# Optimization experiments

Hardware: AMD Instinct MI355X
Metric: run time of the kernel (lower is better)

The kernel has to match this reference:

```python
import jax, jax.numpy as jnp
import numpy as np

EPS = 1e-3  # Keras LayerNormalization default epsilon


def layernorm(x, g, b):
    mu = jnp.mean(x, axis=-1, keepdims=True)
    var = jnp.var(x, axis=-1, keepdims=True)
    return (x - mu) * jax.lax.rsqrt(var + EPS) * g + b


def setup_inputs() -> dict:
    key = jax.random.key(0)
    ks = jax.random.split(key, 16)
    B, T, C = 2, 2048, 1024
    F = 4 * C
    std = 0.02
    inp = {
        "x": jax.random.normal(ks[0], (B, T, C), jnp.float32),
        "ln1_g": jnp.ones((C,), jnp.float32),
        "ln1_b": jnp.zeros((C,), jnp.float32),
        "Wq": std * jax.random.normal(ks[1], (C, C), jnp.float32),
        "bq": jnp.zeros((C,), jnp.float32),
        "Wk": std * jax.random.normal(ks[2], (C, C), jnp.float32),
        "bk": jnp.zeros((C,), jnp.float32),
        "Wv": std * jax.random.normal(ks[3], (C, C), jnp.float32),
        "bv": jnp.zeros((C,), jnp.float32),
        "ln2_g": jnp.ones((C,), jnp.float32),
        "ln2_b": jnp.zeros((C,), jnp.float32),
        "W1": std * jax.random.normal(ks[4], (C, F), jnp.float32),
        "b1": jnp.zeros((F,), jnp.float32),
        "W2": std * jax.random.normal(ks[5], (F, C), jnp.float32),
        "b2": jnp.zeros((C,), jnp.float32),
    }
    return inp


N_HEADS = 16


def reference(x, ln1_g, ln1_b, Wq, bq, Wk, bk, Wv, bv, ln2_g, ln2_b, W1, b1, W2, b2):
    B, T, C = x.shape
    H = N_HEADS
    D = C // H

    h = layernorm(x, ln1_g, ln1_b)
    # [B,T,C] -> [B,H,T,D]
    def split_heads(y):
        return y.reshape(B, T, H, D).transpose(0, 2, 1, 3)

    q = split_heads(h @ Wq + bq)
    k = split_heads(h @ Wk + bk)
    v = split_heads(h @ Wv + bv)

    # Faithful to original: scores = K @ Q^T, i.e. scores[i,j] = k_i . q_j
    scores = jnp.einsum("bhid,bhjd->bhij", k, q) / jnp.sqrt(jnp.float32(D))
    causal = jnp.tril(jnp.ones((T, T), bool))  # [T,T]
    scores = jnp.where(causal[None, None], scores, -jnp.inf)
    w = jax.nn.softmax(scores, axis=-1)
    attn = jnp.einsum("bhij,bhjd->bhid", w, v)  # [B,H,T,D]
    attn = attn.transpose(0, 2, 1, 3).reshape(B, T, C)
    x = x + attn

    h2 = layernorm(x, ln2_g, ln2_b)
    ffn = jax.nn.gelu(h2 @ W1 + b1, approximate=False) @ W2 + b2
    x = x + ffn
    return x
```

## Files before the change

kernel.cpp:

```cpp
#include <hip/hip_runtime.h>
#include <hip/hip_bf16.h>
#include <math.h>

typedef __hip_bfloat16 bf16;
typedef __attribute__((ext_vector_type(8))) short bf16x8;
typedef __attribute__((ext_vector_type(4))) float f32x4;

__device__ __forceinline__ unsigned short f2bf_rne(float f) {
  unsigned u = __float_as_uint(f);
  u += 0x7fffu + ((u >> 16) & 1u);
  return (unsigned short)(u >> 16);
}
__device__ __forceinline__ float bf2f(unsigned short s) {
  return __uint_as_float(((unsigned)s) << 16);
}

__device__ __forceinline__ float gelu_fast(float v) {
  float u = v * (0.7978845608f + 0.0356774081f * v * v);
  float t = __builtin_amdgcn_exp2f(u * 2.8853900818f);
  float r = __builtin_amdgcn_rcpf(t + 1.0f);
  return v - v * r;
}

#define GLOBAL_AS __attribute__((address_space(1)))
#define LDS_AS __attribute__((address_space(3)))
__device__ __forceinline__ void gl2lds16(const void* g, void* l) {
  __builtin_amdgcn_global_load_lds((const GLOBAL_AS void*)g, (LDS_AS void*)l, 16, 0, 0);
}

__device__ __forceinline__ int swz8(int f, int nwg) {
  return (f & 7) * (nwg >> 3) + (f >> 3);
}

#define SCALE_CS 0.18033688011112042f

__device__ __forceinline__ void ln_body(const float* __restrict__ x,
                                        const float* __restrict__ g,
                                        const float* __restrict__ b,
                                        bf16* __restrict__ h, int row, int t) {
  const float4 xv = ((const float4*)(x + (size_t)row * 1024))[t];
  float s = xv.x + xv.y + xv.z + xv.w;
  float sq = xv.x * xv.x + xv.y * xv.y + xv.z * xv.z + xv.w * xv.w;
  #pragma unroll
  for (int m = 1; m < 64; m <<= 1) { s += __shfl_xor(s, m); sq += __shfl_xor(sq, m); }
  __shared__ float ps[4], pq[4];
  if ((t & 63) == 0) { ps[t >> 6] = s; pq[t >> 6] = sq; }
  __syncthreads();
  s = ps[0] + ps[1] + ps[2] + ps[3];
  sq = pq[0] + pq[1] + pq[2] + pq[3];
  float mean = s * (1.0f / 1024.0f);
  float var = sq * (1.0f / 1024.0f) - mean * mean;
  float rs = rsqrtf(var + 1e-3f);
  float4 gv = ((const float4*)g)[t];
  float4 bv = ((const float4*)b)[t];
  ushort4 o;
  o.x = f2bf_rne((xv.x - mean) * rs * gv.x + bv.x);
  o.y = f2bf_rne((xv.y - mean) * rs * gv.y + bv.y);
  o.z = f2bf_rne((xv.z - mean) * rs * gv.z + bv.z);
  o.w = f2bf_rne((xv.w - mean) * rs * gv.w + bv.w);
  ((ushort4*)(h + (size_t)row * 1024))[t] = o;
}

__global__ __launch_bounds__(256) void ln_kernel(const float* __restrict__ x,
                                                 const float* __restrict__ g,
                                                 const float* __restrict__ b,
                                                 bf16* __restrict__ h) {
  ln_body(x, g, b, h, blockIdx.x, threadIdx.x);
}

__device__ __forceinline__ void tr_tile(const float* __restrict__ W, bf16* __restrict__ WT,
                                        int R, int Cc, int bx, int by, int t) {
  __shared__ float tile[32][33];
  int tx = t & 31, ty = t >> 5;
  #pragma unroll
  for (int k = 0; k < 4; k++) {
    int rr = ty + k * 8;
    tile[rr][tx] = W[(size_t)(by + rr) * Cc + bx + tx];
  }
  __syncthreads();
  unsigned short* out = reinterpret_cast<unsigned short*>(WT);
  #pragma unroll
  for (int k = 0; k < 4; k++) {
    int rr = ty + k * 8;
    out[(size_t)(bx + rr) * R + by + tx] = f2bf_rne(tile[tx][rr]);
  }
}

__global__ __launch_bounds__(256) void prep_fused(const float* __restrict__ x,
                                                  const float* __restrict__ ln1g,
                                                  const float* __restrict__ ln1b,
                                                  bf16* __restrict__ h,
                                                  const float* __restrict__ Wq,
                                                  const float* __restrict__ Wk,
                                                  const float* __restrict__ Wv,
                                                  const float* __restrict__ W1,
                                                  const float* __restrict__ W2,
                                                  bf16* __restrict__ WqkT,
                                                  bf16* __restrict__ W1T,
                                                  bf16* __restrict__ W2T) {
  int id = blockIdx.x, t = threadIdx.x;
  if (id < 4096) { ln_body(x, ln1g, ln1b, h, id, t); return; }
  id -= 4096;
  if (id < 3072) {
    int sect = id >> 10, r = id & 1023;
    const float* W = sect == 0 ? Wq : (sect == 1 ? Wk : Wv);
    bf16* WT = WqkT + (size_t)sect * 1048576;
    tr_tile(W, WT, 1024, 1024, (r & 31) * 32, (r >> 5) * 32, t);
  } else if (id < 7168) {
    int r = id - 3072;
    tr_tile(W1, W1T, 1024, 4096, (r & 127) * 32, (r >> 7) * 32, t);
  } else {
    int r = id - 7168;
    tr_tile(W2, W2T, 4096, 1024, (r & 31) * 32, (r >> 5) * 32, t);
  }
}

__device__ __forceinline__ void mainloop_256(const bf16* __restrict__ A,
                                             const bf16* __restrict__ BT,
                                             int lda, int nk, int m0, int n0,
                                             char* ldsb, int t,
                                             f32x4 (&acc)[8][4]) {
  const int lane = t & 63, wave = t >> 6;
  const int l = lane & 15, quad = lane >> 4;
  const int wm = (wave >> 2) * 128, wn = (wave & 3) * 64;
  const int srow = wave * 8 + (lane >> 3);
  const int scol = ((lane & 7) ^ (lane >> 3)) * 8;
  const int grp0 = (quad ^ (l & 7)) * 16;
  const int grp1 = ((4 + quad) ^ (l & 7)) * 16;

  bf16x8 a[4][2], b01[2][2], b23[2][2];

  auto stA = [&](int buf, int half, int kt) {
    const bf16* s = A + (size_t)(m0 + half * 128 + srow) * lda + kt * 64 + scol;
    char* d = ldsb + buf * 65536 + half * 16384 + wave * 1024;
    gl2lds16(s, d);
    gl2lds16(s + (size_t)64 * lda, d + 8192);
  };
  auto stB = [&](int buf, int half, int kt) {
    const bf16* s = BT + (size_t)(n0 + half * 128 + srow) * lda + kt * 64 + scol;
    char* d = ldsb + buf * 65536 + 32768 + half * 16384 + wave * 1024;
    gl2lds16(s, d);
    gl2lds16(s + (size_t)64 * lda, d + 8192);
  };
  auto rdA = [&](int buf, int mh) {
    const char* base = ldsb + buf * 65536 + (wm + mh * 64 + l) * 128;
    #pragma unroll
    for (int ii = 0; ii < 4; ii++) {
      a[ii][0] = *(const bf16x8*)(base + ii * 2048 + grp0);
      a[ii][1] = *(const bf16x8*)(base + ii * 2048 + grp1);
    }
  };
  auto rdB = [&](int buf, int nh, bf16x8 (&bb)[2][2]) {
    const char* base = ldsb + buf * 65536 + 32768 + (wn + nh * 32 + l) * 128;
    #pragma unroll
    for (int jj = 0; jj < 2; jj++) {
      bb[jj][0] = *(const bf16x8*)(base + jj * 2048 + grp0);
      bb[jj][1] = *(const bf16x8*)(base + jj * 2048 + grp1);
    }
  };
  auto mm4 = [&](int mi, bf16x8 (&bb)[2][2], int nj) {
    #pragma unroll
    for (int ii = 0; ii < 4; ii++)
      #pragma unroll
      for (int jj = 0; jj < 2; jj++) {
        acc[mi + ii][nj + jj] = __builtin_amdgcn_mfma_f32_16x16x32_bf16(
            a[ii][0], bb[jj][0], acc[mi + ii][nj + jj], 0, 0, 0);
        acc[mi + ii][nj + jj] = __builtin_amdgcn_mfma_f32_16x16x32_bf16(
            a[ii][1], bb[jj][1], acc[mi + ii][nj + jj], 0, 0, 0);
      }
  };

#define BARX() __builtin_amdgcn_s_barrier()
#define LGKM0() do { asm volatile("s_waitcnt lgkmcnt(0)" ::: "memory"); \
                     __builtin_amdgcn_sched_barrier(0); } while (0)
#define HALF4(BC, DOA, SAB, SAK, DOB, SBB, SBK, VMN)                      \
  do {                                                                    \
    rdA(BC, 0); rdB(BC, 0, b01);                                          \
    if (DOA) stA(SAB, 0, SAK);                                            \
    BARX(); LGKM0();                                                      \
    __builtin_amdgcn_s_setprio(1); mm4(0, b01, 0);                        \
    __builtin_amdgcn_s_setprio(0); BARX();                                \
    rdB(BC, 1, b23);                                                      \
    if (DOA) stA(SAB, 1, SAK);                                            \
    BARX(); LGKM0();                                                      \
    __builtin_amdgcn_s_setprio(1); mm4(0, b23, 2);                        \
    __builtin_amdgcn_s_setprio(0); BARX();                                \
    rdA(BC, 1);                                                           \
    if (DOB) stB(SBB, 0, SBK);                                            \
    BARX(); LGKM0();                                                      \
    __builtin_amdgcn_s_setprio(1); mm4(4, b01, 0);                        \
    __builtin_amdgcn_s_setprio(0); BARX();                                \
    if (DOB) stB(SBB, 1, SBK);                                            \
    BARX();                                                               \
    __builtin_amdgcn_s_setprio(1); mm4(4, b23, 2);                        \
    __builtin_amdgcn_s_setprio(0);                                        \
    asm volatile("s_waitcnt vmcnt(" VMN ")" ::: "memory");                \
    BARX();                                                               \
  } while (0)

  const int nt = nk >> 6;
  stA(0, 0, 0); stA(0, 1, 0);
  stB(0, 0, 0); stB(0, 1, 0);
  stB(1, 0, 1); stB(1, 1, 1);
  asm volatile("s_waitcnt vmcnt(4)" ::: "memory");
  BARX();
  int tt = 0;
  for (; tt + 2 < nt; tt += 2) {
    HALF4(0, 1, 1, tt + 1, 1, 0, tt + 2, "4");
    HALF4(1, 1, 0, tt + 2, 1, 1, tt + 3, "4");
  }
  HALF4(0, 1, 1, tt + 1, 0, 0, 0, "0");
  HALF4(1, 0, 0, 0, 0, 0, 0, "0");
#undef HALF4
#undef LGKM0
#undef BARX
}

__global__ __launch_bounds__(512, 2) void gemm_ffn1(const bf16* __restrict__ A,
                                                    const bf16* __restrict__ BT,
                                                    const float* __restrict__ bias,
                                                    bf16* __restrict__ out,
                                                    int N, int K) {
  extern __shared__ char lds[];
  int t = threadIdx.x;
  int nf = swz8(blockIdx.x, gridDim.x);
  int n0 = (nf & 15) * 256, m0 = (nf >> 4) * 256;
  f32x4 acc[8][4];
  #pragma unroll
  for (int i = 0; i < 8; i++)
    #pragma unroll
    for (int j = 0; j < 4; j++) acc[i][j] = (f32x4){0.f, 0.f, 0.f, 0.f};
  mainloop_256(A, BT, K, K, m0, n0, lds, t, acc);

  int lane = t & 63, wave = t >> 6;
  int l = lane & 15, quad = lane >> 4;
  int wm = (wave >> 2) * 128, wn = (wave & 3) * 64;
  int r4 = quad * 4;
  unsigned short* os = reinterpret_cast<unsigned short*>(out);
  #pragma unroll
  for (int i = 0; i < 8; i++)
    #pragma unroll
    for (int j = 0; j < 4; j++) {
      int col = n0 + wn + j * 16 + l;
      float bval = bias[col];
      #pragma unroll
      for (int r = 0; r < 4; r++) {
        int row = m0 + wm + i * 16 + r4 + r;
        os[(size_t)row * N + col] = f2bf_rne(gelu_fast(acc[i][j][r] + bval));
      }
    }
}

__global__ __launch_bounds__(512, 2) void gemm_ffn2(const bf16* __restrict__ A,
                                                    const bf16* __restrict__ BT,
                                                    unsigned short* __restrict__ p0,
                                                    unsigned short* __restrict__ p1,
                                                    unsigned short* __restrict__ p2,
                                                    unsigned short* __restrict__ p3) {
  extern __shared__ char lds[];
  int t = threadIdx.x;
  int nf = swz8(blockIdx.x, gridDim.x);
  int n0 = (nf & 3) * 256, m0 = ((nf >> 2) & 15) * 256;
  int z = nf >> 6;
  f32x4 acc[8][4];
  #pragma unroll
  for (int i = 0; i < 8; i++)
    #pragma unroll
    for (int j = 0; j < 4; j++) acc[i][j] = (f32x4){0.f, 0.f, 0.f, 0.f};
  mainloop_256(A + z * 1024, BT + z * 1024, 4096, 1024, m0, n0, lds, t, acc);

  unsigned short* p = z == 0 ? p0 : (z == 1 ? p1 : (z == 2 ? p2 : p3));
  int lane = t & 63, wave = t >> 6;
  int l = lane & 15, quad = lane >> 4;
  int wm = (wave >> 2) * 128, wn = (wave & 3) * 64;
  int r4 = quad * 4;
  #pragma unroll
  for (int i = 0; i < 8; i++)
    #pragma unroll
    for (int j = 0; j < 4; j++) {
      int col = n0 + wn + j * 16 + l;
      #pragma unroll
      for (int r = 0; r < 4; r++) {
        int row = m0 + wm + i * 16 + r4 + r;
        p[(size_t)row * 1024 + col] = f2bf_rne(acc[i][j][r]);
      }
    }
}

__global__ __launch_bounds__(256) void reduce_ffn2(const unsigned short* __restrict__ p0,
                                                   const unsigned short* __restrict__ p1,
                                                   const unsigned short* __restrict__ p2,
                                                   const unsigned short* __restrict__ p3,
                                                   const float* __restrict__ x1,
                                                   const float* __restrict__ bias,
                                                   float* __restrict__ out) {
  int row = blockIdx.x, t = threadIdx.x;
  size_t base = (size_t)row * 1024;
  ushort4 a = ((const ushort4*)(p0 + base))[t];
  ushort4 b = ((const ushort4*)(p1 + base))[t];
  ushort4 c = ((const ushort4*)(p2 + base))[t];
  ushort4 d = ((const ushort4*)(p3 + base))[t];
  float4 xv = ((const float4*)(x1 + base))[t];
  float4 bv = ((const float4*)bias)[t];
  float4 o;
  o.x = (bf2f(a.x) + bf2f(b.x)) + (bf2f(c.x) + bf2f(d.x)) + xv.x + bv.x;
  o.y = (bf2f(a.y) + bf2f(b.y)) + (bf2f(c.y) + bf2f(d.y)) + xv.y + bv.y;
  o.z = (bf2f(a.z) + bf2f(b.z)) + (bf2f(c.z) + bf2f(d.z)) + xv.z + bv.z;
  o.w = (bf2f(a.w) + bf2f(b.w)) + (bf2f(c.w) + bf2f(d.w)) + xv.w + bv.w;
  ((float4*)(out + base))[t] = o;
}

__global__ __launch_bounds__(512, 2) void gemm_qkv(const bf16* __restrict__ A,
                                                   const bf16* __restrict__ BT,
                                                   const float* __restrict__ bq,
                                                   const float* __restrict__ bk,
                                                   const float* __restrict__ bv,
                                                   bf16* __restrict__ qb,
                                                   bf16* __restrict__ kb,
                                                   bf16* __restrict__ vt,
                                                   int K) {
  extern __shared__ char lds[];
  int t = threadIdx.x;
  int nf = swz8(blockIdx.x, gridDim.x);
  int n0 = (nf % 12) * 256, m0 = (nf / 12) * 256;
  f32x4 acc[8][4];
  #pragma unroll
  for (int i = 0; i < 8; i++)
    #pragma unroll
    for (int j = 0; j < 4; j++) acc[i][j] = (f32x4){0.f, 0.f, 0.f, 0.f};
  mainloop_256(A, BT, K, K, m0, n0, lds, t, acc);

  int lane = t & 63, wave = t >> 6;
  int l = lane & 15, quad = lane >> 4;
  int wm = (wave >> 2) * 128, wn = (wave & 3) * 64;
  int sect = n0 >> 10;
  const float* bias = sect == 0 ? bq : (sect == 1 ? bk : bv);
  int r4 = quad * 4;
  if (sect < 2) {
    bf16* o = sect == 0 ? qb : kb;
    unsigned short* os = reinterpret_cast<unsigned short*>(o);
    float scl = sect == 1 ? SCALE_CS : 1.0f;
    #pragma unroll
    for (int i = 0; i < 8; i++)
      #pragma unroll
      for (int j = 0; j < 4; j++) {
        int col = n0 + wn + j * 16 + l;
        int c1 = col & 1023;
        float bval = bias[c1];
        int row0 = m0 + wm + i * 16 + r4;
        #pragma unroll
        for (int r = 0; r < 4; r++)
          os[(size_t)(row0 + r) * 1024 + c1] = f2bf_rne((acc[i][j][r] + bval) * scl);
      }
  } else {
    unsigned short* Ls = (unsigned short*)lds;
    #pragma unroll
    for (int i = 0; i < 8; i++)
      #pragma unroll
      for (int j = 0; j < 4; j++) {
        int c1l = wn + j * 16 + l;
        float bval = bias[(n0 - 2048) + c1l];
        ushort4 pk;
        pk.x = f2bf_rne(acc[i][j][0] + bval);
        pk.y = f2bf_rne(acc[i][j][1] + bval);
        pk.z = f2bf_rne(acc[i][j][2] + bval);
        pk.w = f2bf_rne(acc[i][j][3] + bval);
        int gq = ((wm + i * 16) >> 2) + quad;
        *(ushort4*)((char*)Ls + c1l * 512 + ((gq ^ (c1l & 15)) << 3)) = pk;
      }
    __syncthreads();
    int bb = m0 >> 11, t0b = m0 & 2047;
    size_t vbase = ((size_t)(bb * 1024 + (n0 - 2048))) * 2048 + t0b;
    #pragma unroll 4
    for (int it2 = 0; it2 < 32; it2++) {
      int c1row = it2 * 8 + wave;
      uint2 v = *(const uint2*)((char*)Ls + c1row * 512 +
                                ((lane ^ (c1row & 15)) << 3));
      *(uint2*)((unsigned short*)vt + vbase + (size_t)c1row * 2048 + lane * 4) = v;
    }
  }
}

__global__ __launch_bounds__(512, 4) void attn_mfma(const bf16* __restrict__ qb,
                                                    const bf16* __restrict__ kb,
                                                    const bf16* __restrict__ vt,
                                                    const float* __restrict__ x,
                                                    float* __restrict__ x1) {
  extern __shared__ char alds[];
  char* KVb = alds;
  char* Pb  = alds + 65536;
  int t = threadIdx.x;
  int nf = swz8(blockIdx.x, 1024);
  int chunk = nf >> 7, local = nf & 127;
  int y = local >> 2;
  int bh = chunk * 4 + (local & 3);
  int b = bh >> 4, h = bh & 15;
  size_t qk_base = (size_t)b * 2048 * 1024 + (size_t)h * 64;
  size_t vt_base = (size_t)bh * 64 * 2048;
  int lane = t & 63, wave = t >> 6;
  int g = wave >> 2, w4 = wave & 3;
  int l = lane & 15, quad = lane >> 4;
  int sw = l & 7;
  int srow8 = lane >> 3;
  int scol = ((lane & 7) ^ srow8) * 8;
  int it = 31 - y;
  int i0 = it * 64;
  int njt = it + 1;
  int iblk = i0 + w4 * 16;

  bf16x8 ones;
  #pragma unroll
  for (int z = 0; z < 8; z++) ones[z] = (short)0x3F80;

  if (g == 0) {
    #pragma unroll
    for (int c = 0; c < 2; c++) {
      int rr = w4 * 16 + c * 8 + srow8;
      gl2lds16(kb + qk_base + (size_t)(i0 + rr) * 1024 + scol,
               Pb + w4 * 2048 + c * 1024);
      gl2lds16(qb + qk_base + (size_t)rr * 1024 + scol,
               KVb + w4 * 2048 + c * 1024);
      gl2lds16(vt + vt_base + (size_t)rr * 2048 + scol,
               KVb + 8192 + w4 * 2048 + c * 1024);
    }
  } else if (njt > 1) {
    #pragma unroll
    for (int c = 0; c < 2; c++) {
      int rr = w4 * 16 + c * 8 + srow8;
      gl2lds16(qb + qk_base + (size_t)(64 + rr) * 1024 + scol,
               KVb + 32768 + w4 * 2048 + c * 1024);
      gl2lds16(vt + vt_base + (size_t)rr * 2048 + 64 + scol,
               KVb + 32768 + 8192 + w4 * 2048 + c * 1024);
    }
  }
  __syncthreads();

  const char* qr = Pb + w4 * 2048 + l * 128;
  bf16x8 qf0 = *(const bf16x8*)(qr + ((quad ^ sw) * 16));
  bf16x8 qf1 = *(const bf16x8*)(qr + (((4 + quad) ^ sw) * 16));
  __syncthreads();

  f32x4 Oacc[4], Ol;
  #pragma unroll
  for (int dt = 0; dt < 4; dt++) Oacc[dt] = (f32x4){0.f, 0.f, 0.f, 0.f};
  Ol = (f32x4){0.f, 0.f, 0.f, 0.f};

  char* Pw = Pb + wave * 2048 + l * 128;
  char* KVg = KVb + g * 32768;
  int nstep = (njt + 1) >> 1;
  int buf = 0;
  for (int s = 0; s < nstep; s++) {
    int jt = 2 * s + g;
    if (jt + 2 < njt) {
      int j1 = (jt + 2) * 64;
      #pragma unroll
      for (int c = 0; c < 2; c++) {
        int rr = w4 * 16 + c * 8 + srow8;
        gl2lds16(qb + qk_base + (size_t)(j1 + rr) * 1024 + scol,
                 KVg + (buf ^ 1) * 16384 + w4 * 2048 + c * 1024);
        gl2lds16(vt + vt_base + (size_t)rr * 2048 + j1 + scol,
                 KVg + (buf ^ 1) * 16384 + 8192 + w4 * 2048 + c * 1024);
      }
    }
    if (jt < njt) {
      int j0v = jt * 64;
      const bf16* Kb = (const bf16*)(KVg + buf * 16384);
      #pragma unroll
      for (int nt = 0; nt < 4; nt++) {
        int jb = j0v + nt * 16;
        uint2 pk;
        if (jb > iblk + 15) {
          pk.x = 0u; pk.y = 0u;
        } else {
          const bf16* kr = Kb + (nt * 16 + l) * 64;
          bf16x8 kf0 = *(const bf16x8*)(kr + ((quad ^ sw) * 8));
          bf16x8 kf1 = *(const bf16x8*)(kr + (((4 + quad) ^ sw) * 8));
          f32x4 sv = (f32x4){0.f, 0.f, 0.f, 0.f};
          sv = __builtin_amdgcn_mfma_f32_16x16x32_bf16(kf0, qf0, sv, 0, 0, 0);
          sv = __builtin_amdgcn_mfma_f32_16x16x32_bf16(kf1, qf1, sv, 0, 0, 0);
          float p0, p1, p2, p3;
          if (jb + 15 <= iblk) {
            p0 = __builtin_amdgcn_exp2f(sv[0]);
            p1 = __builtin_amdgcn_exp2f(sv[1]);
            p2 = __builtin_amdgcn_exp2f(sv[2]);
            p3 = __builtin_amdgcn_exp2f(sv[3]);
          } else {
            int i_ = iblk + l, jbase = jb + quad * 4;
            p0 = (jbase + 0 > i_) ? 0.f : __builtin_amdgcn_exp2f(sv[0]);
            p1 = (jbase + 1 > i_) ? 0.f : __builtin_amdgcn_exp2f(sv[1]);
            p2 = (jbase + 2 > i_) ? 0.f : __builtin_amdgcn_exp2f(sv[2]);
            p3 = (jbase + 3 > i_) ? 0.f : __builtin_amdgcn_exp2f(sv[3]);
          }
          union { __hip_bfloat162 h2; unsigned u; } c0u, c1u;
          c0u.h2 = __float22bfloat162_rn(make_float2(p0, p1));
          c1u.h2 = __float22bfloat162_rn(make_float2(p2, p3));
          pk.x = c0u.u; pk.y = c1u.u;
        }
        *(uint2*)(Pw + (((nt * 2 + (quad >> 1)) ^ sw) << 4) + ((quad & 1) << 3)) = pk;
      }
      asm volatile("s_waitcnt lgkmcnt(0)" ::: "memory");

      bf16x8 ap0 = *(const bf16x8*)(Pw + ((quad ^ sw) << 4));
      bf16x8 ap1 = *(const bf16x8*)(Pw + (((4 + quad) ^ sw) << 4));
      const bf16* Vb = (const bf16*)(KVg + buf * 16384 + 8192);
      #pragma unroll
      for (int dt = 0; dt < 4; dt++) {
        const bf16* vr = Vb + (dt * 16 + l) * 64;
        bf16x8 bv0 = *(const bf16x8*)(vr + ((quad ^ sw) * 8));
        bf16x8 bv1 = *(const bf16x8*)(vr + (((4 + quad) ^ sw) * 8));
        Oacc[dt] = __builtin_amdgcn_mfma_f32_16x16x32_bf16(ap0, bv0, Oacc[dt], 0, 0, 0);
        Oacc[dt] = __builtin_amdgcn_mfma_f32_16x16x32_bf16(ap1, bv1, Oacc[dt], 0, 0, 0);
      }
      Ol = __builtin_amdgcn_mfma_f32_16x16x32_bf16(ap0, ones, Ol, 0, 0, 0);
      Ol = __builtin_amdgcn_mfma_f32_16x16x32_bf16(ap1, ones, Ol, 0, 0, 0);
    }
    __syncthreads();
    buf ^= 1;
  }

  float* F = (float*)KVb;
  int fbase = w4 * 1280;
  if (g == 1) {
    #pragma unroll
    for (int dt = 0; dt < 4; dt++)
      #pragma unroll
      for (int r = 0; r < 4; r++)
        F[fbase + (dt * 4 + r) * 64 + lane] = Oacc[dt][r];
    #pragma unroll
    for (int r = 0; r < 4; r++)
      F[fbase + 1024 + r * 64 + lane] = Ol[r];
  }
  __syncthreads();
  if (g == 0) {
    #pragma unroll
    for (int dt = 0; dt < 4; dt++)
      #pragma unroll
      for (int r = 0; r < 4; r++)
        Oacc[dt][r] += F[fbase + (dt * 4 + r) * 64 + lane];
    #pragma unroll
    for (int r = 0; r < 4; r++)
      Ol[r] += F[fbase + 1024 + r * 64 + lane];
    #pragma unroll
    for (int r = 0; r < 4; r++) {
      float inv = 1.0f / Ol[r];
      int row = iblk + quad * 4 + r;
      size_t gi = qk_base + (size_t)row * 1024;
      #pragma unroll
      for (int dt = 0; dt < 4; dt++) {
        int d = dt * 16 + l;
        x1[gi + d] = x[gi + d] + Oacc[dt][r] * inv;
      }
    }
  }
}

extern "C" void kernel_launch(void* const* d_in, const int* in_sizes, int n_in,
                              void* d_out, int out_size, void* d_ws, size_t ws_size,
                              hipStream_t stream) {
  const float* x    = (const float*)d_in[0];
  const float* ln1g = (const float*)d_in[1];
  const float* ln1b = (const float*)d_in[2];
  const float* Wq   = (const float*)d_in[3];
  const float* bq   = (const float*)d_in[4];
  const float* Wk   = (const float*)d_in[5];
  const float* bk   = (const float*)d_in[6];
  const float* Wv   = (const float*)d_in[7];
  const float* bv   = (const float*)d_in[8];
  const float* ln2g = (const float*)d_in[9];
  const float* ln2b = (const float*)d_in[10];
  const float* W1   = (const float*)d_in[11];
  const float* b1   = (const float*)d_in[12];
  const float* W2   = (const float*)d_in[13];
  const float* b2   = (const float*)d_in[14];

  char* ws = (char*)d_ws;
  float* x1  = (float*)(ws + 0);
  bf16* h    = (bf16*)(ws + 16777216);
  bf16* WqkT = (bf16*)(ws + 25165824);
  bf16* W1T  = (bf16*)(ws + 31457280);
  bf16* W2T  = (bf16*)(ws + 39845888);
  bf16* qb   = (bf16*)(ws + 48234496);
  bf16* kb   = (bf16*)(ws + 56623104);
  bf16* vt   = (bf16*)(ws + 65011712);
  bf16* act  = (bf16*)(ws + 73400320);

  static bool s_attr_done = false;
  if (!s_attr_done) {
    hipFuncSetAttribute(reinterpret_cast<const void*>(gemm_qkv),
                        hipFuncAttributeMaxDynamicSharedMemorySize, 131072);
    hipFuncSetAttribute(reinterpret_cast<const void*>(gemm_ffn1),
                        hipFuncAttributeMaxDynamicSharedMemorySize, 131072);
    hipFuncSetAttribute(reinterpret_cast<const void*>(gemm_ffn2),
                        hipFuncAttributeMaxDynamicSharedMemorySize, 131072);
    hipFuncSetAttribute(reinterpret_cast<const void*>(attn_mfma),
                        hipFuncAttributeMaxDynamicSharedMemorySize, 81920);
    s_attr_done = true;
  }

  prep_fused<<<15360, 256, 0, stream>>>(x, ln1g, ln1b, h,
                                        Wq, Wk, Wv, W1, W2, WqkT, W1T, W2T);
  gemm_qkv<<<192, 512, 131072, stream>>>(h, WqkT, bq, bk, bv, qb, kb, vt, 1024);
  attn_mfma<<<1024, 512, 81920, stream>>>(qb, kb, vt, x, x1);
  ln_kernel<<<4096, 256, 0, stream>>>(x1, ln2g, ln2b, h);
  gemm_ffn1<<<256, 512, 131072, stream>>>(h, W1T, b1, act, 4096, 1024);
  gemm_ffn2<<<256, 512, 131072, stream>>>(act, W2T,
      (unsigned short*)qb, (unsigned short*)kb, (unsigned short*)vt, (unsigned short*)h);
  reduce_ffn2<<<4096, 256, 0, stream>>>((const unsigned short*)qb, (const unsigned short*)kb,
                                        (const unsigned short*)vt, (const unsigned short*)h,
                                        x1, b2, (float*)d_out);
}
```

Baseline: 276.4 us.

## Use 256x128 tiles with split-K 2 for FFN2 instead of split-K 4

```diff
diff --git a/kernel.cpp b/kernel.cpp
--- a/kernel.cpp
+++ b/kernel.cpp
@@ -216,6 +216,101 @@
 #undef BARX
 }
 
+__device__ __forceinline__ void mainloop_256x128(const bf16* __restrict__ A,
+                                                 const bf16* __restrict__ BT,
+                                                 int lda, int nk, int m0, int n0,
+                                                 char* ldsb, int t,
+                                                 f32x4 (&acc)[8][2]) {
+  const int lane = t & 63, wave = t >> 6;
+  const int l = lane & 15, quad = lane >> 4;
+  const int wm = (wave >> 2) * 128, wn = (wave & 3) * 32;
+  const int srow = wave * 8 + (lane >> 3);
+  const int scol = ((lane & 7) ^ (lane >> 3)) * 8;
+  const int grp0 = (quad ^ (l & 7)) * 16;
+  const int grp1 = ((4 + quad) ^ (l & 7)) * 16;
+
+  bf16x8 a[4][2], bb[2][2];
+
+  auto stA = [&](int buf, int half, int kt) {
+    const bf16* s = A + (size_t)(m0 + half * 128 + srow) * lda + kt * 64 + scol;
+    char* d = ldsb + buf * 49152 + half * 16384 + wave * 1024;
+    gl2lds16(s, d);
+    gl2lds16(s + (size_t)64 * lda, d + 8192);
+  };
+  auto stB = [&](int buf, int kt) {
+    const bf16* s = BT + (size_t)(n0 + srow) * lda + kt * 64 + scol;
+    char* d = ldsb + buf * 49152 + 32768 + wave * 1024;
+    gl2lds16(s, d);
+    gl2lds16(s + (size_t)64 * lda, d + 8192);
+  };
+  auto rdA = [&](int buf, int mh) {
+    const char* base = ldsb + buf * 49152 + (wm + mh * 64 + l) * 128;
+    #pragma unroll
+    for (int ii = 0; ii < 4; ii++) {
+      a[ii][0] = *(const bf16x8*)(base + ii * 2048 + grp0);
+      a[ii][1] = *(const bf16x8*)(base + ii * 2048 + grp1);
+    }
+  };
+  auto rdB = [&](int buf) {
+    const char* base = ldsb + buf * 49152 + 32768 + (wn + l) * 128;
+    #pragma unroll
+    for (int jj = 0; jj < 2; jj++) {
+      bb[jj][0] = *(const bf16x8*)(base + jj * 2048 + grp0);
+      bb[jj][1] = *(const bf16x8*)(base + jj * 2048 + grp1);
+    }
+  };
+  auto mm = [&](int mi) {
+    #pragma unroll
+    for (int ii = 0; ii < 4; ii++)
+      #pragma unroll
+      for (int jj = 0; jj < 2; jj++) {
+        acc[mi + ii][jj] = __builtin_amdgcn_mfma_f32_16x16x32_bf16(
+            a[ii][0], bb[jj][0], acc[mi + ii][jj], 0, 0, 0);
+        acc[mi + ii][jj] = __builtin_amdgcn_mfma_f32_16x16x32_bf16(
+            a[ii][1], bb[jj][1], acc[mi + ii][jj], 0, 0, 0);
+      }
+  };
+
+#define BARX() __builtin_amdgcn_s_barrier()
+#define LGKM0() do { asm volatile("s_waitcnt lgkmcnt(0)" ::: "memory"); \
+                     __builtin_amdgcn_sched_barrier(0); } while (0)
+  const int nt = nk >> 6;
+  stB(0, 0);
+  stA(0, 0, 0); stA(0, 1, 0);
+  stB(1, 1);
+  asm volatile("s_waitcnt vmcnt(2)" ::: "memory");
+  BARX();
+  for (int T = 0; T < nt; T += 2) {
+    int lastm = (T + 2 >= nt);
+    rdA(0, 0); rdB(0);
+    stA(1, 0, T + 1); stA(1, 1, T + 1);
+    BARX(); LGKM0();
+    __builtin_amdgcn_s_setprio(1); mm(0); __builtin_amdgcn_s_setprio(0);
+    BARX();
+    rdA(0, 1);
+    if (!lastm) stB(0, T + 2);
+    BARX(); LGKM0();
+    __builtin_amdgcn_s_setprio(1); mm(4); __builtin_amdgcn_s_setprio(0);
+    if (!lastm) asm volatile("s_waitcnt vmcnt(2)" ::: "memory");
+    else        asm volatile("s_waitcnt vmcnt(0)" ::: "memory");
+    BARX();
+    rdA(1, 0); rdB(1);
+    if (!lastm) { stA(0, 0, T + 2); stA(0, 1, T + 2); }
+    BARX(); LGKM0();
+    __builtin_amdgcn_s_setprio(1); mm(0); __builtin_amdgcn_s_setprio(0);
+    BARX();
+    rdA(1, 1);
+    if (!lastm) stB(1, T + 3);
+    BARX(); LGKM0();
+    __builtin_amdgcn_s_setprio(1); mm(4); __builtin_amdgcn_s_setprio(0);
+    if (!lastm) asm volatile("s_waitcnt vmcnt(2)" ::: "memory");
+    else        asm volatile("s_waitcnt vmcnt(0)" ::: "memory");
+    BARX();
+  }
+#undef LGKM0
+#undef BARX
+}
+
 __global__ __launch_bounds__(512, 2) void gemm_ffn1(const bf16* __restrict__ A,
                                                     const bf16* __restrict__ BT,
                                                     const float* __restrict__ bias,
@@ -254,30 +349,28 @@
 __global__ __launch_bounds__(512, 2) void gemm_ffn2(const bf16* __restrict__ A,
                                                     const bf16* __restrict__ BT,
                                                     unsigned short* __restrict__ p0,
-                                                    unsigned short* __restrict__ p1,
-                                                    unsigned short* __restrict__ p2,
-                                                    unsigned short* __restrict__ p3) {
+                                                    unsigned short* __restrict__ p1) {
   extern __shared__ char lds[];
   int t = threadIdx.x;
   int nf = swz8(blockIdx.x, gridDim.x);
-  int n0 = (nf & 3) * 256, m0 = ((nf >> 2) & 15) * 256;
-  int z = nf >> 6;
-  f32x4 acc[8][4];
+  int n0 = (nf & 7) * 128, m0 = ((nf >> 3) & 15) * 256;
+  int z = nf >> 7;
+  f32x4 acc[8][2];
   #pragma unroll
   for (int i = 0; i < 8; i++)
     #pragma unroll
-    for (int j = 0; j < 4; j++) acc[i][j] = (f32x4){0.f, 0.f, 0.f, 0.f};
-  mainloop_256(A + z * 1024, BT + z * 1024, 4096, 1024, m0, n0, lds, t, acc);
-
-  unsigned short* p = z == 0 ? p0 : (z == 1 ? p1 : (z == 2 ? p2 : p3));
+    for (int j = 0; j < 2; j++) acc[i][j] = (f32x4){0.f, 0.f, 0.f, 0.f};
+  mainloop_256x128(A + z * 2048, BT + z * 2048, 4096, 2048, m0, n0, lds, t, acc);
+
+  unsigned short* p = z ? p1 : p0;
   int lane = t & 63, wave = t >> 6;
   int l = lane & 15, quad = lane >> 4;
-  int wm = (wave >> 2) * 128, wn = (wave & 3) * 64;
+  int wm = (wave >> 2) * 128, wn = (wave & 3) * 32;
   int r4 = quad * 4;
   #pragma unroll
   for (int i = 0; i < 8; i++)
     #pragma unroll
-    for (int j = 0; j < 4; j++) {
+    for (int j = 0; j < 2; j++) {
       int col = n0 + wn + j * 16 + l;
       #pragma unroll
       for (int r = 0; r < 4; r++) {
@@ -289,8 +382,6 @@
 
 __global__ __launch_bounds__(256) void reduce_ffn2(const unsigned short* __restrict__ p0,
                                                    const unsigned short* __restrict__ p1,
-                                                   const unsigned short* __restrict__ p2,
-                                                   const unsigned short* __restrict__ p3,
                                                    const float* __restrict__ x1,
                                                    const float* __restrict__ bias,
                                                    float* __restrict__ out) {
@@ -298,15 +389,13 @@
   size_t base = (size_t)row * 1024;
   ushort4 a = ((const ushort4*)(p0 + base))[t];
   ushort4 b = ((const ushort4*)(p1 + base))[t];
-  ushort4 c = ((const ushort4*)(p2 + base))[t];
-  ushort4 d = ((const ushort4*)(p3 + base))[t];
   float4 xv = ((const float4*)(x1 + base))[t];
   float4 bv = ((const float4*)bias)[t];
   float4 o;
-  o.x = (bf2f(a.x) + bf2f(b.x)) + (bf2f(c.x) + bf2f(d.x)) + xv.x + bv.x;
-  o.y = (bf2f(a.y) + bf2f(b.y)) + (bf2f(c.y) + bf2f(d.y)) + xv.y + bv.y;
-  o.z = (bf2f(a.z) + bf2f(b.z)) + (bf2f(c.z) + bf2f(d.z)) + xv.z + bv.z;
-  o.w = (bf2f(a.w) + bf2f(b.w)) + (bf2f(c.w) + bf2f(d.w)) + xv.w + bv.w;
+  o.x = (bf2f(a.x) + bf2f(b.x)) + xv.x + bv.x;
+  o.y = (bf2f(a.y) + bf2f(b.y)) + xv.y + bv.y;
+  o.z = (bf2f(a.z) + bf2f(b.z)) + xv.z + bv.z;
+  o.w = (bf2f(a.w) + bf2f(b.w)) + xv.w + bv.w;
   ((float4*)(out + base))[t] = o;
 }
 
@@ -591,7 +680,7 @@
     hipFuncSetAttribute(reinterpret_cast<const void*>(gemm_ffn1),
                         hipFuncAttributeMaxDynamicSharedMemorySize, 131072);
     hipFuncSetAttribute(reinterpret_cast<const void*>(gemm_ffn2),
-                        hipFuncAttributeMaxDynamicSharedMemorySize, 131072);
+                        hipFuncAttributeMaxDynamicSharedMemorySize, 98304);
     hipFuncSetAttribute(reinterpret_cast<const void*>(attn_mfma),
                         hipFuncAttributeMaxDynamicSharedMemorySize, 81920);
     s_attr_done = true;
@@ -603,9 +692,8 @@
   attn_mfma<<<1024, 512, 81920, stream>>>(qb, kb, vt, x, x1);
   ln_kernel<<<4096, 256, 0, stream>>>(x1, ln2g, ln2b, h);
   gemm_ffn1<<<256, 512, 131072, stream>>>(h, W1T, b1, act, 4096, 1024);
-  gemm_ffn2<<<256, 512, 131072, stream>>>(act, W2T,
-      (unsigned short*)qb, (unsigned short*)kb, (unsigned short*)vt, (unsigned short*)h);
+  gemm_ffn2<<<256, 512, 98304, stream>>>(act, W2T,
+      (unsigned short*)qb, (unsigned short*)kb);
   reduce_ffn2<<<4096, 256, 0, stream>>>((const unsigned short*)qb, (const unsigned short*)kb,
-                                        (const unsigned short*)vt, (const unsigned short*)h,
                                         x1, b2, (float*)d_out);
 }
```

Result: no change. 275.8 us (-0.2%).

## Replace split-K FFN2 with 128x128 full-K tiles and fused residual epilogue

Applied to the files above, without the earlier changes.

```diff
diff --git a/kernel.cpp b/kernel.cpp
--- a/kernel.cpp
+++ b/kernel.cpp
@@ -216,6 +216,81 @@
 #undef BARX
 }
 
+__device__ __forceinline__ void mainloop_128(const bf16* __restrict__ A,
+                                             const bf16* __restrict__ BT,
+                                             int lda, int nk, int m0, int n0,
+                                             char* ldsb, int t,
+                                             f32x4 (&acc)[4][2]) {
+  const int lane = t & 63, wave = t >> 6;
+  const int l = lane & 15, quad = lane >> 4;
+  const int wm = (wave >> 2) * 64, wn = (wave & 3) * 32;
+  const int srow = wave * 8 + (lane >> 3);
+  const int scol = ((lane & 7) ^ (lane >> 3)) * 8;
+  const int grp0 = (quad ^ (l & 7)) * 16;
+  const int grp1 = ((4 + quad) ^ (l & 7)) * 16;
+
+  bf16x8 a[4][2], bb[2][2];
+
+  auto stage = [&](int buf, int kt) {
+    const bf16* sa = A + (size_t)(m0 + srow) * lda + kt * 64 + scol;
+    char* da = ldsb + buf * 32768 + wave * 1024;
+    gl2lds16(sa, da);
+    gl2lds16(sa + (size_t)64 * lda, da + 8192);
+    const bf16* sb = BT + (size_t)(n0 + srow) * lda + kt * 64 + scol;
+    char* db = ldsb + buf * 32768 + 16384 + wave * 1024;
+    gl2lds16(sb, db);
+    gl2lds16(sb + (size_t)64 * lda, db + 8192);
+  };
+  auto rd = [&](int buf) {
+    const char* ab = ldsb + buf * 32768 + (wm + l) * 128;
+    #pragma unroll
+    for (int ii = 0; ii < 4; ii++) {
+      a[ii][0] = *(const bf16x8*)(ab + ii * 2048 + grp0);
+      a[ii][1] = *(const bf16x8*)(ab + ii * 2048 + grp1);
+    }
+    const char* bbase = ldsb + buf * 32768 + 16384 + (wn + l) * 128;
+    #pragma unroll
+    for (int jj = 0; jj < 2; jj++) {
+      bb[jj][0] = *(const bf16x8*)(bbase + jj * 2048 + grp0);
+      bb[jj][1] = *(const bf16x8*)(bbase + jj * 2048 + grp1);
+    }
+  };
+  auto mm = [&]() {
+    #pragma unroll
+    for (int ii = 0; ii < 4; ii++)
+      #pragma unroll
+      for (int jj = 0; jj < 2; jj++) {
+        acc[ii][jj] = __builtin_amdgcn_mfma_f32_16x16x32_bf16(
+            a[ii][0], bb[jj][0], acc[ii][jj], 0, 0, 0);
+        acc[ii][jj] = __builtin_amdgcn_mfma_f32_16x16x32_bf16(
+            a[ii][1], bb[jj][1], acc[ii][jj], 0, 0, 0);
+      }
+  };
+
+#define BARX() __builtin_amdgcn_s_barrier()
+#define LGKM0() do { asm volatile("s_waitcnt lgkmcnt(0)" ::: "memory"); \
+                     __builtin_amdgcn_sched_barrier(0); } while (0)
+  const int nt = nk >> 6;
+  stage(0, 0);
+  stage(1, 1);
+  asm volatile("s_waitcnt vmcnt(4)" ::: "memory");
+  BARX();
+  int buf = 0;
+  for (int T = 0; T < nt; T++) {
+    rd(buf);
+    int dos = (T + 2 < nt);
+    if (dos) stage((buf + 2) % 3, T + 2);
+    BARX(); LGKM0();
+    __builtin_amdgcn_s_setprio(1); mm(); __builtin_amdgcn_s_setprio(0);
+    if (dos) asm volatile("s_waitcnt vmcnt(4)" ::: "memory");
+    else     asm volatile("s_waitcnt vmcnt(0)" ::: "memory");
+    BARX();
+    buf = buf + 1 == 3 ? 0 : buf + 1;
+  }
+#undef LGKM0
+#undef BARX
+}
+
 __global__ __launch_bounds__(512, 2) void gemm_ffn1(const bf16* __restrict__ A,
                                                     const bf16* __restrict__ BT,
                                                     const float* __restrict__ bias,
@@ -253,61 +328,36 @@
 
 __global__ __launch_bounds__(512, 2) void gemm_ffn2(const bf16* __restrict__ A,
                                                     const bf16* __restrict__ BT,
-                                                    unsigned short* __restrict__ p0,
-                                                    unsigned short* __restrict__ p1,
-                                                    unsigned short* __restrict__ p2,
-                                                    unsigned short* __restrict__ p3) {
+                                                    const float* __restrict__ x1,
+                                                    const float* __restrict__ bias,
+                                                    float* __restrict__ out) {
   extern __shared__ char lds[];
   int t = threadIdx.x;
   int nf = swz8(blockIdx.x, gridDim.x);
-  int n0 = (nf & 3) * 256, m0 = ((nf >> 2) & 15) * 256;
-  int z = nf >> 6;
-  f32x4 acc[8][4];
-  #pragma unroll
-  for (int i = 0; i < 8; i++)
-    #pragma unroll
-    for (int j = 0; j < 4; j++) acc[i][j] = (f32x4){0.f, 0.f, 0.f, 0.f};
-  mainloop_256(A + z * 1024, BT + z * 1024, 4096, 1024, m0, n0, lds, t, acc);
-
-  unsigned short* p = z == 0 ? p0 : (z == 1 ? p1 : (z == 2 ? p2 : p3));
+  int n0 = (nf & 7) * 128, m0 = (nf >> 3) * 128;
+  f32x4 acc[4][2];
+  #pragma unroll
+  for (int i = 0; i < 4; i++)
+    #pragma unroll
+    for (int j = 0; j < 2; j++) acc[i][j] = (f32x4){0.f, 0.f, 0.f, 0.f};
+  mainloop_128(A, BT, 4096, 4096, m0, n0, lds, t, acc);
+
   int lane = t & 63, wave = t >> 6;
   int l = lane & 15, quad = lane >> 4;
-  int wm = (wave >> 2) * 128, wn = (wave & 3) * 64;
-  int r4 = quad * 4;
-  #pragma unroll
-  for (int i = 0; i < 8; i++)
-    #pragma unroll
-    for (int j = 0; j < 4; j++) {
+  int wm = (wave >> 2) * 64, wn = (wave & 3) * 32;
+  #pragma unroll
+  for (int i = 0; i < 4; i++)
+    #pragma unroll
+    for (int j = 0; j < 2; j++) {
       int col = n0 + wn + j * 16 + l;
+      float bval = bias[col];
       #pragma unroll
       for (int r = 0; r < 4; r++) {
-        int row = m0 + wm + i * 16 + r4 + r;
-        p[(size_t)row * 1024 + col] = f2bf_rne(acc[i][j][r]);
-      }
-    }
-}
-
-__global__ __launch_bounds__(256) void reduce_ffn2(const unsigned short* __restrict__ p0,
-                                                   const unsigned short* __restrict__ p1,
-                                                   const unsigned short* __restrict__ p2,
-                                                   const unsigned short* __restrict__ p3,
-                                                   const float* __restrict__ x1,
-                                                   const float* __restrict__ bias,
-                                                   float* __restrict__ out) {
-  int row = blockIdx.x, t = threadIdx.x;
-  size_t base = (size_t)row * 1024;
-  ushort4 a = ((const ushort4*)(p0 + base))[t];
-  ushort4 b = ((const ushort4*)(p1 + base))[t];
-  ushort4 c = ((const ushort4*)(p2 + base))[t];
-  ushort4 d = ((const ushort4*)(p3 + base))[t];
-  float4 xv = ((const float4*)(x1 + base))[t];
-  float4 bv = ((const float4*)bias)[t];
-  float4 o;
-  o.x = (bf2f(a.x) + bf2f(b.x)) + (bf2f(c.x) + bf2f(d.x)) + xv.x + bv.x;
-  o.y = (bf2f(a.y) + bf2f(b.y)) + (bf2f(c.y) + bf2f(d.y)) + xv.y + bv.y;
-  o.z = (bf2f(a.z) + bf2f(b.z)) + (bf2f(c.z) + bf2f(d.z)) + xv.z + bv.z;
-  o.w = (bf2f(a.w) + bf2f(b.w)) + (bf2f(c.w) + bf2f(d.w)) + xv.w + bv.w;
-  ((float4*)(out + base))[t] = o;
+        int row = m0 + wm + i * 16 + quad * 4 + r;
+        size_t o = (size_t)row * 1024 + col;
+        out[o] = acc[i][j][r] + x1[o] + bval;
+      }
+    }
 }
 
 __global__ __launch_bounds__(512, 2) void gemm_qkv(const bf16* __restrict__ A,
@@ -591,7 +641,7 @@
     hipFuncSetAttribute(reinterpret_cast<const void*>(gemm_ffn1),
                         hipFuncAttributeMaxDynamicSharedMemorySize, 131072);
     hipFuncSetAttribute(reinterpret_cast<const void*>(gemm_ffn2),
-                        hipFuncAttributeMaxDynamicSharedMemorySize, 131072);
+                        hipFuncAttributeMaxDynamicSharedMemorySize, 98304);
     hipFuncSetAttribute(reinterpret_cast<const void*>(attn_mfma),
                         hipFuncAttributeMaxDynamicSharedMemorySize, 81920);
     s_attr_done = true;
@@ -603,9 +653,5 @@
   attn_mfma<<<1024, 512, 81920, stream>>>(qb, kb, vt, x, x1);
   ln_kernel<<<4096, 256, 0, stream>>>(x1, ln2g, ln2b, h);
   gemm_ffn1<<<256, 512, 131072, stream>>>(h, W1T, b1, act, 4096, 1024);
-  gemm_ffn2<<<256, 512, 131072, stream>>>(act, W2T,
-      (unsigned short*)qb, (unsigned short*)kb, (unsigned short*)vt, (unsigned short*)h);
-  reduce_ffn2<<<4096, 256, 0, stream>>>((const unsigned short*)qb, (const unsigned short*)kb,
-                                        (const unsigned short*)vt, (const unsigned short*)h,
-                                        x1, b2, (float*)d_out);
-}
+  gemm_ffn2<<<256, 512, 98304, stream>>>(act, W2T, x1, b2, (float*)d_out);
+}
```

After: 277.8 us. About the same (+0.5%).
